# Performance work log

Hardware: AMD Instinct MI355X
Metric: run time of the kernel (lower is better)

The kernel has to match this reference:

```python
import jax, jax.numpy as jnp
import numpy as np

N_NODES = 20000
N_EDGES = 320000
IN_CH = 256
HID_CH = 256   # 2 * out_channels
OUT_CH = 128


def gcn_conv(x, edge_index, W, b, n_nodes):
    """PyG GCNConv: linear transform, add self-loops, sym-normalized scatter-add."""
    x = x @ W  # [N, C_out]
    loop = jnp.arange(n_nodes, dtype=edge_index.dtype)
    row = jnp.concatenate([edge_index[0], loop])  # source nodes
    col = jnp.concatenate([edge_index[1], loop])  # destination nodes
    deg = jax.ops.segment_sum(jnp.ones_like(col, dtype=x.dtype), col,
                              num_segments=n_nodes)
    deg_inv_sqrt = jnp.where(deg > 0, jax.lax.rsqrt(deg), 0.0)
    norm = deg_inv_sqrt[row] * deg_inv_sqrt[col]  # [E+N]
    msg = x[row] * norm[:, None]                  # gather + scale
    out = jax.ops.segment_sum(msg, col, num_segments=n_nodes)  # scatter-add
    return out + b


def setup_inputs() -> dict:
    key = jax.random.key(0)
    k1, k2, k3, k4, k5 = jax.random.split(key, 5)
    doc_embeds = jax.random.normal(k1, (N_NODES, IN_CH), dtype=jnp.float32)
    edge_index = jax.random.randint(k2, (2, N_EDGES), 0, N_NODES, dtype=jnp.int64)
    # Glorot-style init for GCN weights, zero bias (PyG defaults)
    s1 = 1.0 / np.sqrt(IN_CH)
    s2 = 1.0 / np.sqrt(HID_CH)
    W1 = jax.random.uniform(k3, (IN_CH, HID_CH), jnp.float32, -s1, s1)
    b1 = jnp.zeros((HID_CH,), jnp.float32)
    W2 = jax.random.uniform(k4, (HID_CH, OUT_CH), jnp.float32, -s2, s2)
    b2 = jnp.zeros((OUT_CH,), jnp.float32)
    return {"doc_embeds": doc_embeds, "edge_index": edge_index,
            "W1": W1, "b1": b1, "W2": W2, "b2": b2}


def reference(doc_embeds, edge_index, W1, b1, W2, b2):
    n = doc_embeds.shape[0]
    x = jax.nn.relu(gcn_conv(doc_embeds, edge_index, W1, b1, n))
    x = gcn_conv(x, edge_index, W2, b2, n)
    return x
```

## Files before the change

kernel.cpp:

```cpp
#include <hip/hip_runtime.h>
#include <math.h>

#define N_NODES 20000
#define N_EDGES 320000
#define IN_CH   256
#define HID_CH  256
#define OUT_CH  128
#define CAP     64

typedef __attribute__((ext_vector_type(8))) short short8;
typedef __attribute__((ext_vector_type(8))) unsigned short ushort8;
typedef __attribute__((ext_vector_type(4))) unsigned short ushort4v;
typedef __attribute__((ext_vector_type(4))) float floatx4;

static __device__ __forceinline__ unsigned short f2bf(float f) {
    unsigned int u = __float_as_uint(f);
    u += 0x7FFFu + ((u >> 16) & 1u);
    return (unsigned short)(u >> 16);
}
static __device__ __forceinline__ float bf2f(unsigned short h) {
    return __uint_as_float(((unsigned int)h) << 16);
}

__global__ __launch_bounds__(256)
void init_kernel(const float* __restrict__ W1, const float* __restrict__ W2,
                 unsigned short* __restrict__ W1thi, unsigned short* __restrict__ W1tlo,
                 unsigned short* __restrict__ W2thi, unsigned short* __restrict__ W2tlo,
                 int* __restrict__ deg) {
    const int g = blockIdx.x * blockDim.x + threadIdx.x;
    const int gsz = gridDim.x * blockDim.x;
    for (int i = g; i < N_NODES; i += gsz) deg[i] = 0;
    for (int i = g; i < IN_CH * HID_CH; i += gsz) {
        int k = i / HID_CH, n = i % HID_CH;
        float x = W1[i];
        unsigned short h = f2bf(x);
        unsigned short l = f2bf(x - bf2f(h));
        W1thi[(size_t)n * IN_CH + k] = h;
        W1tlo[(size_t)n * IN_CH + k] = l;
    }
    for (int i = g; i < HID_CH * OUT_CH; i += gsz) {
        int k = i / OUT_CH, n = i % OUT_CH;
        float x = W2[i];
        unsigned short h = f2bf(x);
        unsigned short l = f2bf(x - bf2f(h));
        W2thi[(size_t)n * HID_CH + k] = h;
        W2tlo[(size_t)n * HID_CH + k] = l;
    }
}

__global__ void degfill_kernel(const int* __restrict__ row, const int* __restrict__ col,
                               int* __restrict__ deg, unsigned short* __restrict__ srcs, int E) {
    int i = blockIdx.x * blockDim.x + threadIdx.x;
    if (i < E) {
        int c = col[i];
        int r = row[i];
        int p = atomicAdd(&deg[c], 1);
        srcs[(size_t)c * CAP + p] = (unsigned short)r;
    }
}

#define GK 256
template <int AFP32, int TM>
__global__ __launch_bounds__(256)
void gemm_mfma_kernel(const float* __restrict__ Afp,
                      const unsigned short* __restrict__ Ahi, const unsigned short* __restrict__ Alo,
                      const unsigned short* __restrict__ Bthi, const unsigned short* __restrict__ Btlo,
                      const int* __restrict__ deg, float* __restrict__ C, int M, int N) {
    constexpr int MI = TM / 32;
    __shared__ unsigned short As[2][TM][36];
    __shared__ unsigned short Bs[2][128][36];
    const int tid = threadIdx.x;
    const int m0 = blockIdx.y * TM;
    const int n0 = blockIdx.x * 128;
    const int lane = tid & 63;
    const int wave = tid >> 6;
    const int wr = (wave >> 1) * (TM / 2);
    const int wc = (wave & 1) * 64;
    const int lm = lane & 15;
    const int lk = (lane >> 4) * 8;

    floatx4 acc[MI][4];
#pragma unroll
    for (int i = 0; i < MI; ++i)
#pragma unroll
        for (int j = 0; j < 4; ++j) acc[i][j] = (floatx4){0.f, 0.f, 0.f, 0.f};

    for (int k0 = 0; k0 < GK; k0 += 32) {
#pragma unroll
        for (int c = 0; c < TM / 64; ++c) {
            int ch = tid + c * 256;
            int r = ch >> 2;
            int ko = (ch & 3) * 8;
            ushort8 vh = {}, vl = {};
            if (m0 + r < M) {
                if (AFP32) {
                    const float* ap = Afp + (size_t)(m0 + r) * GK + k0 + ko;
                    float4 f0 = *(const float4*)ap;
                    float4 f1 = *(const float4*)(ap + 4);
                    float xs[8] = {f0.x, f0.y, f0.z, f0.w, f1.x, f1.y, f1.z, f1.w};
#pragma unroll
                    for (int j = 0; j < 8; ++j) {
                        vh[j] = f2bf(xs[j]);
                        vl[j] = f2bf(xs[j] - bf2f(vh[j]));
                    }
                } else {
                    size_t ga = (size_t)(m0 + r) * GK + k0 + ko;
                    vh = *(const ushort8*)(Ahi + ga);
                    vl = *(const ushort8*)(Alo + ga);
                }
            }
            *(ushort8*)&As[0][r][ko] = vh;
            *(ushort8*)&As[1][r][ko] = vl;
        }
#pragma unroll
        for (int c = 0; c < 2; ++c) {
            int ch = tid + c * 256;
            int r = ch >> 2;
            int ko = (ch & 3) * 8;
            size_t gb = (size_t)(n0 + r) * GK + k0 + ko;
            *(ushort8*)&Bs[0][r][ko] = *(const ushort8*)(Bthi + gb);
            *(ushort8*)&Bs[1][r][ko] = *(const ushort8*)(Btlo + gb);
        }
        __syncthreads();

        short8 ah[MI], al[MI], bh[4], bl[4];
#pragma unroll
        for (int i = 0; i < MI; ++i) {
            ah[i] = *(const short8*)&As[0][wr + i * 16 + lm][lk];
            al[i] = *(const short8*)&As[1][wr + i * 16 + lm][lk];
        }
#pragma unroll
        for (int j = 0; j < 4; ++j) {
            bh[j] = *(const short8*)&Bs[0][wc + j * 16 + lm][lk];
            bl[j] = *(const short8*)&Bs[1][wc + j * 16 + lm][lk];
        }
#pragma unroll
        for (int i = 0; i < MI; ++i)
#pragma unroll
            for (int j = 0; j < 4; ++j) {
                acc[i][j] = __builtin_amdgcn_mfma_f32_16x16x32_bf16(ah[i], bh[j], acc[i][j], 0, 0, 0);
                acc[i][j] = __builtin_amdgcn_mfma_f32_16x16x32_bf16(ah[i], bl[j], acc[i][j], 0, 0, 0);
                acc[i][j] = __builtin_amdgcn_mfma_f32_16x16x32_bf16(al[i], bh[j], acc[i][j], 0, 0, 0);
            }
        __syncthreads();
    }

#pragma unroll
    for (int i = 0; i < MI; ++i) {
#pragma unroll
        for (int r = 0; r < 4; ++r) {
            int rowi = m0 + wr + i * 16 + (lane >> 4) * 4 + r;
            if (rowi < M) {
                float dr = 1.0f / sqrtf((float)(deg[rowi] + 1));
#pragma unroll
                for (int j = 0; j < 4; ++j) {
                    C[(size_t)rowi * N + n0 + wc + j * 16 + lm] = dr * acc[i][j][r];
                }
            }
        }
    }
}

template <int C, int NSLICE, int MODE>
__global__ __launch_bounds__(256)
void gather_sliced_kernel(const float* __restrict__ X, const int* __restrict__ deg,
                          const unsigned short* __restrict__ srcs,
                          const float* __restrict__ bias, float* __restrict__ outf,
                          unsigned short* __restrict__ outhi, unsigned short* __restrict__ outlo,
                          int n) {
    constexpr int SW  = C / NSLICE;
    constexpr int L   = SW / 4;
    constexpr int NPW = 64 / L;
    const int slice = blockIdx.x % NSLICE;
    const int ngrp  = blockIdx.x / NSLICE;
    const int wave = threadIdx.x >> 6;
    const int lane = threadIdx.x & 63;
    const int g  = lane / L;
    const int sl = lane % L;
    const int node = ngrp * (4 * NPW) + wave * NPW + g;
    if (node >= n) return;
    const int choff = slice * SW + sl * 4;
    const size_t beg = (size_t)node * CAP;
    const int cnt = deg[node];

    float4 acc = make_float4(0.f, 0.f, 0.f, 0.f);
    int e = 0;
    for (; e + 4 <= cnt; e += 4) {
        ushort4v s4 = *(const ushort4v*)(srcs + beg + e);
        float4 v0 = *(const float4*)(X + (size_t)s4.x * C + choff);
        float4 v1 = *(const float4*)(X + (size_t)s4.y * C + choff);
        float4 v2 = *(const float4*)(X + (size_t)s4.z * C + choff);
        float4 v3 = *(const float4*)(X + (size_t)s4.w * C + choff);
        acc.x += v0.x + v1.x + v2.x + v3.x;
        acc.y += v0.y + v1.y + v2.y + v3.y;
        acc.z += v0.z + v1.z + v2.z + v3.z;
        acc.w += v0.w + v1.w + v2.w + v3.w;
    }
    for (; e < cnt; ++e) {
        int r = srcs[beg + e];
        float4 v = *(const float4*)(X + (size_t)r * C + choff);
        acc.x += v.x; acc.y += v.y; acc.z += v.z; acc.w += v.w;
    }

    const float dc = 1.0f / sqrtf((float)(cnt + 1));
    float4 vs = *(const float4*)(X + (size_t)node * C + choff);
    float4 bb = *(const float4*)(bias + choff);

    float o0 = dc * (acc.x + vs.x) + bb.x;
    float o1 = dc * (acc.y + vs.y) + bb.y;
    float o2 = dc * (acc.z + vs.z) + bb.z;
    float o3 = dc * (acc.w + vs.w) + bb.w;

    if constexpr (MODE == 1) {
        o0 = fmaxf(o0, 0.f); o1 = fmaxf(o1, 0.f);
        o2 = fmaxf(o2, 0.f); o3 = fmaxf(o3, 0.f);
        ushort4v h, l;
        h.x = f2bf(o0); l.x = f2bf(o0 - bf2f(h.x));
        h.y = f2bf(o1); l.y = f2bf(o1 - bf2f(h.y));
        h.z = f2bf(o2); l.z = f2bf(o2 - bf2f(h.z));
        h.w = f2bf(o3); l.w = f2bf(o3 - bf2f(h.w));
        __builtin_nontemporal_store(h, (ushort4v*)(outhi + (size_t)node * C + choff));
        __builtin_nontemporal_store(l, (ushort4v*)(outlo + (size_t)node * C + choff));
    } else {
        floatx4 o = {o0, o1, o2, o3};
        __builtin_nontemporal_store(o, (floatx4*)(outf + (size_t)node * C + choff));
    }
}

extern "C" void kernel_launch(void* const* d_in, const int* in_sizes, int n_in,
                              void* d_out, int out_size, void* d_ws, size_t ws_size,
                              hipStream_t stream) {
    const float* doc_embeds = (const float*)d_in[0];
    const int*   edge_index = (const int*)d_in[1];
    const float* W1 = (const float*)d_in[2];
    const float* b1 = (const float*)d_in[3];
    const float* W2 = (const float*)d_in[4];
    const float* b2 = (const float*)d_in[5];
    float* out = (float*)d_out;

    const int* row = edge_index;
    const int* col = edge_index + N_EDGES;

    char* ws = (char*)d_ws;
    auto align_up = [](size_t x) { return (x + 255) / 256 * 256; };

    float*          X1s  = (float*)(ws);
    unsigned short* H1hi = (unsigned short*)(ws + align_up((size_t)N_NODES * HID_CH * 4));
    unsigned short* H1lo = H1hi + (size_t)N_NODES * HID_CH;
    float*          X2s  = X1s;
    char* meta = (char*)(H1lo + (size_t)N_NODES * HID_CH);
    unsigned short* W1thi = (unsigned short*)(meta); meta += align_up((size_t)IN_CH * HID_CH * 2);
    unsigned short* W1tlo = (unsigned short*)(meta); meta += align_up((size_t)IN_CH * HID_CH * 2);
    unsigned short* W2thi = (unsigned short*)(meta); meta += align_up((size_t)HID_CH * OUT_CH * 2);
    unsigned short* W2tlo = (unsigned short*)(meta); meta += align_up((size_t)HID_CH * OUT_CH * 2);
    int*            deg   = (int*)(meta);            meta += align_up((size_t)N_NODES * 4);
    unsigned short* srcs  = (unsigned short*)(meta);

    init_kernel<<<256, 256, 0, stream>>>(W1, W2, W1thi, W1tlo, W2thi, W2tlo, deg);
    degfill_kernel<<<(N_EDGES + 255) / 256, 256, 0, stream>>>(row, col, deg, srcs, N_EDGES);

    {
        dim3 grid(HID_CH / 128, (N_NODES + 63) / 64);
        gemm_mfma_kernel<1, 64><<<grid, 256, 0, stream>>>(
            doc_embeds, nullptr, nullptr, W1thi, W1tlo, deg, X1s, N_NODES, HID_CH);
    }
    gather_sliced_kernel<HID_CH, 8, 1><<<((N_NODES + 31) / 32) * 8, 256, 0, stream>>>(
        X1s, deg, srcs, b1, nullptr, H1hi, H1lo, N_NODES);

    {
        dim3 grid(OUT_CH / 128, (N_NODES + 63) / 64);
        gemm_mfma_kernel<0, 64><<<grid, 256, 0, stream>>>(
            nullptr, H1hi, H1lo, W2thi, W2tlo, deg, X2s, N_NODES, OUT_CH);
    }
    gather_sliced_kernel<OUT_CH, 8, 0><<<((N_NODES + 63) / 64) * 8, 256, 0, stream>>>(
        X2s, deg, srcs, b2, out, nullptr, nullptr, N_NODES);
}
```

Before: 184.3 us.

## Store intermediate GEMM outputs in fp16 to halve gather traffic

The GEMM epilogue now writes the degree-scaled features as fp16 instead of fp32, and both gather kernels read half4 rows and accumulate in fp32, halving the bytes moved by the random-access neighbor gathers. The gather kernel is fixed to 32-channel slices, so the second layer now uses 4 slices. The weight split/transpose init is vectorised, and the layer-1 hi/lo stores are switched from nontemporal to regular stores. The fp16 intermediates add rounding error compared with the previous fp32 path.

Result: faster. 177.7 us (-3.6%).

```diff
diff --git a/kernel.cpp b/kernel.cpp
--- a/kernel.cpp
+++ b/kernel.cpp
@@ -12,6 +12,7 @@
 typedef __attribute__((ext_vector_type(8))) unsigned short ushort8;
 typedef __attribute__((ext_vector_type(4))) unsigned short ushort4v;
 typedef __attribute__((ext_vector_type(4))) float floatx4;
+typedef __attribute__((ext_vector_type(4))) _Float16 half4;
 
 static __device__ __forceinline__ unsigned short f2bf(float f) {
     unsigned int u = __float_as_uint(f);
@@ -30,21 +31,37 @@
     const int g = blockIdx.x * blockDim.x + threadIdx.x;
     const int gsz = gridDim.x * blockDim.x;
     for (int i = g; i < N_NODES; i += gsz) deg[i] = 0;
-    for (int i = g; i < IN_CH * HID_CH; i += gsz) {
-        int k = i / HID_CH, n = i % HID_CH;
-        float x = W1[i];
-        unsigned short h = f2bf(x);
-        unsigned short l = f2bf(x - bf2f(h));
-        W1thi[(size_t)n * IN_CH + k] = h;
-        W1tlo[(size_t)n * IN_CH + k] = l;
-    }
-    for (int i = g; i < HID_CH * OUT_CH; i += gsz) {
-        int k = i / OUT_CH, n = i % OUT_CH;
-        float x = W2[i];
-        unsigned short h = f2bf(x);
-        unsigned short l = f2bf(x - bf2f(h));
-        W2thi[(size_t)n * HID_CH + k] = h;
-        W2tlo[(size_t)n * HID_CH + k] = l;
+    for (int t = g; t < (IN_CH * HID_CH) / 16; t += gsz) {
+        int n = t >> 4;
+        int kc = (t & 15) * 16;
+        ushort8 h0, l0, h1, l1;
+#pragma unroll
+        for (int j = 0; j < 8; ++j) {
+            float x = W1[(size_t)(kc + j) * HID_CH + n];
+            h0[j] = f2bf(x); l0[j] = f2bf(x - bf2f(h0[j]));
+            float y = W1[(size_t)(kc + 8 + j) * HID_CH + n];
+            h1[j] = f2bf(y); l1[j] = f2bf(y - bf2f(h1[j]));
+        }
+        *(ushort8*)(W1thi + (size_t)n * IN_CH + kc)     = h0;
+        *(ushort8*)(W1thi + (size_t)n * IN_CH + kc + 8) = h1;
+        *(ushort8*)(W1tlo + (size_t)n * IN_CH + kc)     = l0;
+        *(ushort8*)(W1tlo + (size_t)n * IN_CH + kc + 8) = l1;
+    }
+    for (int t = g; t < (HID_CH * OUT_CH) / 16; t += gsz) {
+        int n = t >> 4;
+        int kc = (t & 15) * 16;
+        ushort8 h0, l0, h1, l1;
+#pragma unroll
+        for (int j = 0; j < 8; ++j) {
+            float x = W2[(size_t)(kc + j) * OUT_CH + n];
+            h0[j] = f2bf(x); l0[j] = f2bf(x - bf2f(h0[j]));
+            float y = W2[(size_t)(kc + 8 + j) * OUT_CH + n];
+            h1[j] = f2bf(y); l1[j] = f2bf(y - bf2f(h1[j]));
+        }
+        *(ushort8*)(W2thi + (size_t)n * HID_CH + kc)     = h0;
+        *(ushort8*)(W2thi + (size_t)n * HID_CH + kc + 8) = h1;
+        *(ushort8*)(W2tlo + (size_t)n * HID_CH + kc)     = l0;
+        *(ushort8*)(W2tlo + (size_t)n * HID_CH + kc + 8) = l1;
     }
 }
 
@@ -65,7 +82,7 @@
 void gemm_mfma_kernel(const float* __restrict__ Afp,
                       const unsigned short* __restrict__ Ahi, const unsigned short* __restrict__ Alo,
                       const unsigned short* __restrict__ Bthi, const unsigned short* __restrict__ Btlo,
-                      const int* __restrict__ deg, float* __restrict__ C, int M, int N) {
+                      const int* __restrict__ deg, _Float16* __restrict__ C, int M, int N) {
     constexpr int MI = TM / 32;
     __shared__ unsigned short As[2][TM][36];
     __shared__ unsigned short Bs[2][128][36];
@@ -154,7 +171,7 @@
                 float dr = 1.0f / sqrtf((float)(deg[rowi] + 1));
 #pragma unroll
                 for (int j = 0; j < 4; ++j) {
-                    C[(size_t)rowi * N + n0 + wc + j * 16 + lm] = dr * acc[i][j][r];
+                    C[(size_t)rowi * N + n0 + wc + j * 16 + lm] = (_Float16)(dr * acc[i][j][r]);
                 }
             }
         }
@@ -163,21 +180,20 @@
 
 template <int C, int NSLICE, int MODE>
 __global__ __launch_bounds__(256)
-void gather_sliced_kernel(const float* __restrict__ X, const int* __restrict__ deg,
+void gather_sliced_kernel(const _Float16* __restrict__ X, const int* __restrict__ deg,
                           const unsigned short* __restrict__ srcs,
                           const float* __restrict__ bias, float* __restrict__ outf,
                           unsigned short* __restrict__ outhi, unsigned short* __restrict__ outlo,
                           int n) {
-    constexpr int SW  = C / NSLICE;
-    constexpr int L   = SW / 4;
-    constexpr int NPW = 64 / L;
+    constexpr int SW = C / NSLICE;
+    static_assert(SW == 32, "slice must be 32 channels");
     const int slice = blockIdx.x % NSLICE;
     const int ngrp  = blockIdx.x / NSLICE;
     const int wave = threadIdx.x >> 6;
     const int lane = threadIdx.x & 63;
-    const int g  = lane / L;
-    const int sl = lane % L;
-    const int node = ngrp * (4 * NPW) + wave * NPW + g;
+    const int g  = lane >> 3;
+    const int sl = lane & 7;
+    const int node = ngrp * 32 + wave * 8 + g;
     if (node >= n) return;
     const int choff = slice * SW + sl * 4;
     const size_t beg = (size_t)node * CAP;
@@ -187,29 +203,30 @@
     int e = 0;
     for (; e + 4 <= cnt; e += 4) {
         ushort4v s4 = *(const ushort4v*)(srcs + beg + e);
-        float4 v0 = *(const float4*)(X + (size_t)s4.x * C + choff);
-        float4 v1 = *(const float4*)(X + (size_t)s4.y * C + choff);
-        float4 v2 = *(const float4*)(X + (size_t)s4.z * C + choff);
-        float4 v3 = *(const float4*)(X + (size_t)s4.w * C + choff);
-        acc.x += v0.x + v1.x + v2.x + v3.x;
-        acc.y += v0.y + v1.y + v2.y + v3.y;
-        acc.z += v0.z + v1.z + v2.z + v3.z;
-        acc.w += v0.w + v1.w + v2.w + v3.w;
+        half4 v0 = *(const half4*)(X + (size_t)s4.x * C + choff);
+        half4 v1 = *(const half4*)(X + (size_t)s4.y * C + choff);
+        half4 v2 = *(const half4*)(X + (size_t)s4.z * C + choff);
+        half4 v3 = *(const half4*)(X + (size_t)s4.w * C + choff);
+        acc.x += (float)v0.x + (float)v1.x + (float)v2.x + (float)v3.x;
+        acc.y += (float)v0.y + (float)v1.y + (float)v2.y + (float)v3.y;
+        acc.z += (float)v0.z + (float)v1.z + (float)v2.z + (float)v3.z;
+        acc.w += (float)v0.w + (float)v1.w + (float)v2.w + (float)v3.w;
     }
     for (; e < cnt; ++e) {
         int r = srcs[beg + e];
-        float4 v = *(const float4*)(X + (size_t)r * C + choff);
-        acc.x += v.x; acc.y += v.y; acc.z += v.z; acc.w += v.w;
+        half4 v = *(const half4*)(X + (size_t)r * C + choff);
+        acc.x += (float)v.x; acc.y += (float)v.y;
+        acc.z += (float)v.z; acc.w += (float)v.w;
     }
 
     const float dc = 1.0f / sqrtf((float)(cnt + 1));
-    float4 vs = *(const float4*)(X + (size_t)node * C + choff);
+    half4 vsh = *(const half4*)(X + (size_t)node * C + choff);
     float4 bb = *(const float4*)(bias + choff);
 
-    float o0 = dc * (acc.x + vs.x) + bb.x;
-    float o1 = dc * (acc.y + vs.y) + bb.y;
-    float o2 = dc * (acc.z + vs.z) + bb.z;
-    float o3 = dc * (acc.w + vs.w) + bb.w;
+    float o0 = dc * (acc.x + (float)vsh.x) + bb.x;
+    float o1 = dc * (acc.y + (float)vsh.y) + bb.y;
+    float o2 = dc * (acc.z + (float)vsh.z) + bb.z;
+    float o3 = dc * (acc.w + (float)vsh.w) + bb.w;
 
     if constexpr (MODE == 1) {
         o0 = fmaxf(o0, 0.f); o1 = fmaxf(o1, 0.f);
@@ -219,8 +236,8 @@
         h.y = f2bf(o1); l.y = f2bf(o1 - bf2f(h.y));
         h.z = f2bf(o2); l.z = f2bf(o2 - bf2f(h.z));
         h.w = f2bf(o3); l.w = f2bf(o3 - bf2f(h.w));
-        __builtin_nontemporal_store(h, (ushort4v*)(outhi + (size_t)node * C + choff));
-        __builtin_nontemporal_store(l, (ushort4v*)(outlo + (size_t)node * C + choff));
+        *(ushort4v*)(outhi + (size_t)node * C + choff) = h;
+        *(ushort4v*)(outlo + (size_t)node * C + choff) = l;
     } else {
         floatx4 o = {o0, o1, o2, o3};
         __builtin_nontemporal_store(o, (floatx4*)(outf + (size_t)node * C + choff));
@@ -244,10 +261,10 @@
     char* ws = (char*)d_ws;
     auto align_up = [](size_t x) { return (x + 255) / 256 * 256; };
 
-    float*          X1s  = (float*)(ws);
-    unsigned short* H1hi = (unsigned short*)(ws + align_up((size_t)N_NODES * HID_CH * 4));
+    _Float16*       X1s  = (_Float16*)(ws);
+    unsigned short* H1hi = (unsigned short*)(ws + align_up((size_t)N_NODES * HID_CH * 2));
     unsigned short* H1lo = H1hi + (size_t)N_NODES * HID_CH;
-    float*          X2s  = X1s;
+    _Float16*       X2s  = X1s;
     char* meta = (char*)(H1lo + (size_t)N_NODES * HID_CH);
     unsigned short* W1thi = (unsigned short*)(meta); meta += align_up((size_t)IN_CH * HID_CH * 2);
     unsigned short* W1tlo = (unsigned short*)(meta); meta += align_up((size_t)IN_CH * HID_CH * 2);
@@ -272,6 +289,6 @@
         gemm_mfma_kernel<0, 64><<<grid, 256, 0, stream>>>(
             nullptr, H1hi, H1lo, W2thi, W2tlo, deg, X2s, N_NODES, OUT_CH);
     }
-    gather_sliced_kernel<OUT_CH, 8, 0><<<((N_NODES + 63) / 64) * 8, 256, 0, stream>>>(
+    gather_sliced_kernel<OUT_CH, 4, 0><<<((N_NODES + 31) / 32) * 4, 256, 0, stream>>>(
         X2s, deg, srcs, b2, out, nullptr, nullptr, N_NODES);
 }
```
